# Optimization experiments

Measured on AMD Instinct MI355X. Metric: run time of the kernel, lower is better.

The kernel has to match this reference:

```python
import jax, jax.numpy as jnp
import numpy as np

H = 4096          # hidden_size
I = 14336         # intermediate_size
G = 128           # quantization group size along the input dim


def dequant(q, s, g=G):
    """Dequantize group-scaled int4 weights.
    q: [out, in] int (values in [-8, 7]); s: [out, in//g] float scales.
    Returns fp weight [out, in]: W[o, i] = q[o, i] * s[o, i // g].
    """
    O, In = q.shape
    return (q.reshape(O, In // g, g).astype(s.dtype) * s[:, :, None]).reshape(O, In)


def setup_inputs() -> dict:
    key = jax.random.key(0)
    ks = jax.random.split(key, 7)
    x = jax.random.normal(ks[0], (2, 2048, H), dtype=jnp.float32)

    def mk_qlinear(kq, ksc, out_d, in_d):
        q = jax.random.randint(kq, (out_d, in_d), -8, 8, dtype=jnp.int32)  # int4 range
        s = jax.random.uniform(ksc, (out_d, in_d // G), dtype=jnp.float32,
                               minval=0.005, maxval=0.02)
        return q, s

    gate_q, gate_s = mk_qlinear(ks[1], ks[2], I, H)
    up_q, up_s = mk_qlinear(ks[3], ks[4], I, H)
    down_q, down_s = mk_qlinear(ks[5], ks[6], H, I)
    return {"x": x,
            "gate_q": gate_q, "gate_s": gate_s,
            "up_q": up_q, "up_s": up_s,
            "down_q": down_q, "down_s": down_s}


def reference(x, gate_q, gate_s, up_q, up_s, down_q, down_s):
    # SwiGLU MLP: down( silu(gate(x)) * up(x) ) with group-dequantized weights.
    Wg = dequant(gate_q, gate_s)   # [I, H]
    Wu = dequant(up_q, up_s)       # [I, H]
    Wd = dequant(down_q, down_s)   # [H, I]
    gate_score = jax.nn.silu(jnp.einsum('bsh,ih->bsi', x, Wg))
    intermediate = gate_score * jnp.einsum('bsh,ih->bsi', x, Wu)
    return jnp.einsum('bsi,hi->bsh', intermediate, Wd)
```

## Files before the change

kernel.cpp:

```cpp
#include <hip/hip_runtime.h>
#include <hip/hip_bf16.h>


#define HDIM 4096
#define IDIM 14336
#define MTOK 4096
#define GRP 128

typedef __attribute__((ext_vector_type(8))) short bf16x8;
typedef __attribute__((ext_vector_type(4))) float f32x4;
typedef __attribute__((ext_vector_type(4))) unsigned short u16x4;

#define WAIT_LGKM0 asm volatile("s_waitcnt lgkmcnt(0)" ::: "memory")
#define WAIT_VM(N) asm volatile("s_waitcnt vmcnt(" #N ")" ::: "memory")
#define SBAR       __builtin_amdgcn_s_barrier()
#define SCHB       __builtin_amdgcn_sched_barrier(0)

__device__ __forceinline__ unsigned short f2bf(float f) {
  union { float f; unsigned int u; } v; v.f = f;
  return (unsigned short)((v.u + 0x7fffu + ((v.u >> 16) & 1u)) >> 16);
}
__device__ __forceinline__ unsigned pk2(float a, float b) {
  union { float f; unsigned u; } ua, ub; ua.f = a; ub.f = b;
  return __builtin_amdgcn_perm(ub.u, ua.u, 0x07060302u);
}

#define GLD16(G, L)                                                           \
  __builtin_amdgcn_global_load_lds(                                           \
      (const __attribute__((address_space(1))) unsigned int*)(G),             \
      (__attribute__((address_space(3))) unsigned int*)(L), 16, 0, 0)

__global__ __launch_bounds__(256) void cvt_x_kernel(const float* __restrict__ x,
                                                    unsigned short* __restrict__ xb) {
  const int n = MTOK * HDIM;
  const int stride = gridDim.x * 256 * 4;
  for (int i = (blockIdx.x * 256 + threadIdx.x) * 4; i < n; i += stride) {
    float4 v = *reinterpret_cast<const float4*>(x + i);
    u16x4 o;
    o[0] = f2bf(v.x); o[1] = f2bf(v.y); o[2] = f2bf(v.z); o[3] = f2bf(v.w);
    *reinterpret_cast<u16x4*>(xb + i) = o;
  }
}

__global__ __launch_bounds__(256) void deq_kernel(const int* __restrict__ q,
                                                  const float* __restrict__ s,
                                                  unsigned short* __restrict__ w,
                                                  int In) {
  const int row  = blockIdx.y;
  const int col0 = blockIdx.x * 2048 + threadIdx.x * 8;
  const long base = (long)row * In + col0;
  const float sc = s[row * (In / GRP) + (col0 >> 7)];
  const int4* p = (const int4*)(q + base);
  int4 a0 = p[0], a1 = p[1];
  uint4 o;
  o.x = pk2((float)a0.x * sc, (float)a0.y * sc);
  o.y = pk2((float)a0.z * sc, (float)a0.w * sc);
  o.z = pk2((float)a1.x * sc, (float)a1.y * sc);
  o.w = pk2((float)a1.z * sc, (float)a1.w * sc);
  *(uint4*)(w + base) = o;
}

__global__ __launch_bounds__(512, 2) void gateup_bf16(
    const unsigned short* __restrict__ xb,
    const unsigned short* __restrict__ wg,
    const unsigned short* __restrict__ wu,
    unsigned short* __restrict__ inter)
{
  __shared__ unsigned short As[3 * 256 * 64];
  __shared__ unsigned short Bgs[2 * 128 * 64];
  __shared__ unsigned short Bus[2 * 128 * 64];

  const int tid = threadIdx.x, lane = tid & 63, wid = tid >> 6;
  const int wm = wid >> 1, wn = wid & 1;
  const int p = blockIdx.x;
  const int l = (p & 7) * 224 + (p >> 3);
  const int m0 = (l & 15) * 256, n0 = (l >> 4) * 128;
  const int lr = lane & 15, lc = lane >> 4;

  const int ra   = tid >> 3;
  const int scol = ((tid & 7) ^ (ra & 7)) << 3;
  const unsigned short* pa  = xb + (long)(m0 + ra) * HDIM + scol;
  const unsigned short* pbg = wg + (long)(n0 + ra) * HDIM + scol;
  const unsigned short* pbu = wu + (long)(n0 + ra) * HDIM + scol;

#define A1(KT, BUF, IT)                                                       \
  GLD16(pa + (long)(IT) * 64 * HDIM + (long)(KT) * 64,                        \
        (unsigned short*)As + (BUF) * 16384 + (IT) * 4096 + wid * 512)
#define BG1(KT, BUF, IT)                                                      \
  GLD16(pbg + (long)(IT) * 64 * HDIM + (long)(KT) * 64,                       \
        (unsigned short*)Bgs + (BUF) * 8192 + (IT) * 4096 + wid * 512)
#define BU1(KT, BUF, IT)                                                      \
  GLD16(pbu + (long)(IT) * 64 * HDIM + (long)(KT) * 64,                       \
        (unsigned short*)Bus + (BUF) * 8192 + (IT) * 4096 + wid * 512)

  f32x4 accg[4][4], accu[4][4];
  const f32x4 zero = {0.f, 0.f, 0.f, 0.f};
#pragma unroll
  for (int i = 0; i < 4; ++i)
#pragma unroll
    for (int j = 0; j < 4; ++j) { accg[i][j] = zero; accu[i][j] = zero; }

  A1(0, 0, 0); A1(0, 0, 1); A1(0, 0, 2); A1(0, 0, 3);
  SCHB;
  BG1(0, 0, 0); BG1(0, 0, 1); BU1(0, 0, 0); BU1(0, 0, 1);
  SCHB;
  A1(1, 1, 0); A1(1, 1, 1); A1(1, 1, 2); A1(1, 1, 3);
  SCHB;

  const int NK = HDIM / 64;
#pragma unroll 1
  for (int kt = 0; kt < NK; ++kt) {
    WAIT_VM(4);
    SCHB;
    SBAR;
    SCHB;
    const unsigned short* Ab  = (const unsigned short*)As  + (kt % 3) * 16384;
    const unsigned short* Bgb = (const unsigned short*)Bgs + (kt & 1) * 8192;
    const unsigned short* Bub = (const unsigned short*)Bus + (kt & 1) * 8192;
    const int ktb = (kt + 1 < NK) ? kt + 1 : NK - 1;
    const int wrb = (kt + 1) & 1;
    const int kta = (kt + 2 < NK) ? kt + 2 : NK - 1;
    const int wra = (kt + 2) % 3;
    const int soff0 = (lc ^ (lr & 7)) << 3;
    const int soff1 = ((4 + lc) ^ (lr & 7)) << 3;
    bf16x8 af[4], bfr[4];

#pragma unroll
    for (int mi = 0; mi < 4; ++mi)
      af[mi] = *(const bf16x8*)&Ab[(wm * 64 + mi * 16 + lr) * 64 + soff0];
#pragma unroll
    for (int ni = 0; ni < 4; ++ni)
      bfr[ni] = *(const bf16x8*)&Bgb[(wn * 64 + ni * 16 + lr) * 64 + soff0];
    BG1(ktb, wrb, 0); BG1(ktb, wrb, 1);
    SCHB; SBAR; WAIT_LGKM0; SCHB;
    __builtin_amdgcn_s_setprio(1);
#pragma unroll
    for (int ni = 0; ni < 4; ++ni)
#pragma unroll
      for (int mi = 0; mi < 4; ++mi)
        accg[mi][ni] = __builtin_amdgcn_mfma_f32_16x16x32_bf16(af[mi], bfr[ni], accg[mi][ni], 0, 0, 0);
    __builtin_amdgcn_s_setprio(0);

#pragma unroll
    for (int ni = 0; ni < 4; ++ni)
      bfr[ni] = *(const bf16x8*)&Bub[(wn * 64 + ni * 16 + lr) * 64 + soff0];
    BU1(ktb, wrb, 0); BU1(ktb, wrb, 1);
    SCHB; SBAR; WAIT_LGKM0; SCHB;
    __builtin_amdgcn_s_setprio(1);
#pragma unroll
    for (int ni = 0; ni < 4; ++ni)
#pragma unroll
      for (int mi = 0; mi < 4; ++mi)
        accu[mi][ni] = __builtin_amdgcn_mfma_f32_16x16x32_bf16(af[mi], bfr[ni], accu[mi][ni], 0, 0, 0);
    __builtin_amdgcn_s_setprio(0);

#pragma unroll
    for (int mi = 0; mi < 4; ++mi)
      af[mi] = *(const bf16x8*)&Ab[(wm * 64 + mi * 16 + lr) * 64 + soff1];
#pragma unroll
    for (int ni = 0; ni < 4; ++ni)
      bfr[ni] = *(const bf16x8*)&Bgb[(wn * 64 + ni * 16 + lr) * 64 + soff1];
    A1(kta, wra, 0); A1(kta, wra, 1);
    SCHB; SBAR; WAIT_LGKM0; SCHB;
    __builtin_amdgcn_s_setprio(1);
#pragma unroll
    for (int ni = 0; ni < 4; ++ni)
#pragma unroll
      for (int mi = 0; mi < 4; ++mi)
        accg[mi][ni] = __builtin_amdgcn_mfma_f32_16x16x32_bf16(af[mi], bfr[ni], accg[mi][ni], 0, 0, 0);
    __builtin_amdgcn_s_setprio(0);

#pragma unroll
    for (int ni = 0; ni < 4; ++ni)
      bfr[ni] = *(const bf16x8*)&Bub[(wn * 64 + ni * 16 + lr) * 64 + soff1];
    A1(kta, wra, 2); A1(kta, wra, 3);
    SCHB; SBAR; WAIT_LGKM0; SCHB;
    __builtin_amdgcn_s_setprio(1);
#pragma unroll
    for (int ni = 0; ni < 4; ++ni)
#pragma unroll
      for (int mi = 0; mi < 4; ++mi)
        accu[mi][ni] = __builtin_amdgcn_mfma_f32_16x16x32_bf16(af[mi], bfr[ni], accu[mi][ni], 0, 0, 0);
    __builtin_amdgcn_s_setprio(0);
    SCHB;
  }

  const int r0 = m0 + wm * 64, c0 = n0 + wn * 64;
#pragma unroll
  for (int mi = 0; mi < 4; ++mi)
#pragma unroll
    for (int ni = 0; ni < 4; ++ni)
#pragma unroll
      for (int r = 0; r < 4; ++r) {
        float g = accg[mi][ni][r], u = accu[mi][ni][r];
        float sv = g / (1.f + __expf(-g));
        int row = r0 + mi * 16 + lc * 4 + r;
        int col = c0 + ni * 16 + lr;
        inter[(long)row * IDIM + col] = f2bf(sv * u);
      }
#undef A1
#undef BG1
#undef BU1
}

__global__ __launch_bounds__(512, 2) void down_bf16(
    const unsigned short* __restrict__ inter,
    const unsigned short* __restrict__ wd,
    float* __restrict__ out)
{
  __shared__ unsigned short As[2 * 256 * 64];
  __shared__ unsigned short Bs[2 * 256 * 64];

  const int tid = threadIdx.x, lane = tid & 63, wid = tid >> 6;
  const int wm = wid >> 2, wn = wid & 3;
  const int p = blockIdx.x;
  const int l = (p & 7) * 32 + (p >> 3);
  const int m0 = (l & 15) * 256, n0 = (l >> 4) * 256;
  const int lr = lane & 15, lc = lane >> 4;

  const int ra   = tid >> 3;
  const int scol = ((tid & 7) ^ (ra & 7)) << 3;
  const unsigned short* pa = inter + (long)(m0 + ra) * IDIM + scol;
  const unsigned short* pb = wd + (long)(n0 + ra) * IDIM + scol;

#define DA1(KT, BUF, IT)                                                      \
  GLD16(pa + (long)(IT) * 64 * IDIM + (long)(KT) * 64,                        \
        (unsigned short*)As + (BUF) * 16384 + (IT) * 4096 + wid * 512)
#define DB1(KT, BUF, IT)                                                      \
  GLD16(pb + (long)(IT) * 64 * IDIM + (long)(KT) * 64,                        \
        (unsigned short*)Bs + (BUF) * 16384 + (IT) * 4096 + wid * 512)

  f32x4 acc[8][4];
  const f32x4 zero = {0.f, 0.f, 0.f, 0.f};
#pragma unroll
  for (int i = 0; i < 8; ++i)
#pragma unroll
    for (int j = 0; j < 4; ++j) acc[i][j] = zero;

  DB1(0, 0, 0); DB1(0, 0, 1); DB1(0, 0, 2); DB1(0, 0, 3);
  DA1(0, 0, 0); DA1(0, 0, 1); DA1(0, 0, 2); DA1(0, 0, 3);
  SCHB;
  WAIT_VM(0);
  SBAR;
  SCHB;

  const int NK = IDIM / 64;
#pragma unroll 1
  for (int kt = 0; kt < NK; ++kt) {
    const int RD = kt & 1, WR = RD ^ 1;
    const int ktn = (kt + 1 < NK) ? kt + 1 : NK - 1;
    const unsigned short* Ab = (const unsigned short*)As + RD * 16384;
    const unsigned short* Bb = (const unsigned short*)Bs + RD * 16384;
    const int soff0 = (lc ^ (lr & 7)) << 3;
    const int soff1 = ((4 + lc) ^ (lr & 7)) << 3;
    bf16x8 af[8], bfr[4];

#pragma unroll
    for (int mi = 0; mi < 8; ++mi)
      af[mi] = *(const bf16x8*)&Ab[(wm * 128 + mi * 16 + lr) * 64 + soff0];
#pragma unroll
    for (int ni = 0; ni < 4; ++ni)
      bfr[ni] = *(const bf16x8*)&Bb[(wn * 64 + ni * 16 + lr) * 64 + soff0];
    DB1(ktn, WR, 0); DB1(ktn, WR, 1); DB1(ktn, WR, 2); DB1(ktn, WR, 3);
    SCHB; WAIT_LGKM0; SCHB;
    __builtin_amdgcn_s_setprio(1);
#pragma unroll
    for (int ni = 0; ni < 4; ++ni)
#pragma unroll
      for (int mi = 0; mi < 8; ++mi)
        acc[mi][ni] = __builtin_amdgcn_mfma_f32_16x16x32_bf16(af[mi], bfr[ni], acc[mi][ni], 0, 0, 0);
    __builtin_amdgcn_s_setprio(0);

#pragma unroll
    for (int mi = 0; mi < 8; ++mi)
      af[mi] = *(const bf16x8*)&Ab[(wm * 128 + mi * 16 + lr) * 64 + soff1];
#pragma unroll
    for (int ni = 0; ni < 4; ++ni)
      bfr[ni] = *(const bf16x8*)&Bb[(wn * 64 + ni * 16 + lr) * 64 + soff1];
    DA1(ktn, WR, 0); DA1(ktn, WR, 1); DA1(ktn, WR, 2); DA1(ktn, WR, 3);
    SCHB; WAIT_LGKM0; SCHB;
    __builtin_amdgcn_s_setprio(1);
#pragma unroll
    for (int ni = 0; ni < 4; ++ni)
#pragma unroll
      for (int mi = 0; mi < 8; ++mi)
        acc[mi][ni] = __builtin_amdgcn_mfma_f32_16x16x32_bf16(af[mi], bfr[ni], acc[mi][ni], 0, 0, 0);
    __builtin_amdgcn_s_setprio(0);

    SCHB;
    WAIT_VM(0);
    SBAR;
    SCHB;
  }

  const int r0 = m0 + wm * 128, c0 = n0 + wn * 64;
#pragma unroll
  for (int mi = 0; mi < 8; ++mi)
#pragma unroll
    for (int ni = 0; ni < 4; ++ni)
#pragma unroll
      for (int r = 0; r < 4; ++r) {
        int row = r0 + mi * 16 + lc * 4 + r;
        int col = c0 + ni * 16 + lr;
        out[(long)row * HDIM + col] = acc[mi][ni][r];
      }
#undef DA1
#undef DB1
}

extern "C" void kernel_launch(void* const* d_in, const int* in_sizes, int n_in,
                              void* d_out, int out_size, void* d_ws, size_t ws_size,
                              hipStream_t stream) {
  const float* x   = (const float*)d_in[0];
  const int*   gq  = (const int*)d_in[1];
  const float* gsc = (const float*)d_in[2];
  const int*   uq  = (const int*)d_in[3];
  const float* usc = (const float*)d_in[4];
  const int*   dq  = (const int*)d_in[5];
  const float* dsc = (const float*)d_in[6];
  float* out = (float*)d_out;

  unsigned short* xb    = (unsigned short*)d_ws;
  unsigned short* inter = xb + (size_t)MTOK * HDIM;
  unsigned short* wgb   = inter + (size_t)MTOK * IDIM;
  unsigned short* wub   = wgb + (size_t)IDIM * HDIM;

  hipLaunchKernelGGL(cvt_x_kernel, dim3(2048), dim3(256), 0, stream, x, xb);
  hipLaunchKernelGGL(deq_kernel, dim3(HDIM / 2048, IDIM), dim3(256), 0, stream,
                     gq, gsc, wgb, HDIM);
  hipLaunchKernelGGL(deq_kernel, dim3(HDIM / 2048, IDIM), dim3(256), 0, stream,
                     uq, usc, wub, HDIM);
  hipLaunchKernelGGL(gateup_bf16, dim3(1792), dim3(512), 0, stream,
                     xb, wgb, wub, inter);
  hipLaunchKernelGGL(deq_kernel, dim3(IDIM / 2048, HDIM), dim3(256), 0, stream,
                     dq, dsc, wgb, IDIM);
  hipLaunchKernelGGL(down_bf16, dim3(256), dim3(512), 0, stream,
                     inter, wgb, out);
}
```

Baseline: 1.412 ms.

## Switch gate/up GEMM to double-buffered A with one barrier per k-step

Replaces the triple-buffered A and staggered prefetch pipeline in the gate/up kernel with plain double buffering. Each k-step now has one wait-for-all plus one barrier instead of four barriers, and gate and up fragments are loaded together so their MFMAs interleave. This cuts barrier overhead and LDS use, which could allow higher occupancy. The cost is that the full vmcnt(0) wait at the end of every iteration leaves less prefetch depth to hide global-load latency.

```diff
diff --git a/kernel.cpp b/kernel.cpp
--- a/kernel.cpp
+++ b/kernel.cpp
@@ -66,7 +66,7 @@
     const unsigned short* __restrict__ wu,
     unsigned short* __restrict__ inter)
 {
-  __shared__ unsigned short As[3 * 256 * 64];
+  __shared__ unsigned short As[2 * 256 * 64];
   __shared__ unsigned short Bgs[2 * 128 * 64];
   __shared__ unsigned short Bus[2 * 128 * 64];
 
@@ -100,88 +100,68 @@
 #pragma unroll
     for (int j = 0; j < 4; ++j) { accg[i][j] = zero; accu[i][j] = zero; }
 
+  BG1(0, 0, 0); BG1(0, 0, 1); BU1(0, 0, 0); BU1(0, 0, 1);
   A1(0, 0, 0); A1(0, 0, 1); A1(0, 0, 2); A1(0, 0, 3);
   SCHB;
-  BG1(0, 0, 0); BG1(0, 0, 1); BU1(0, 0, 0); BU1(0, 0, 1);
-  SCHB;
-  A1(1, 1, 0); A1(1, 1, 1); A1(1, 1, 2); A1(1, 1, 3);
+  WAIT_VM(0);
+  SBAR;
   SCHB;
 
   const int NK = HDIM / 64;
 #pragma unroll 1
   for (int kt = 0; kt < NK; ++kt) {
-    WAIT_VM(4);
-    SCHB;
-    SBAR;
-    SCHB;
-    const unsigned short* Ab  = (const unsigned short*)As  + (kt % 3) * 16384;
-    const unsigned short* Bgb = (const unsigned short*)Bgs + (kt & 1) * 8192;
-    const unsigned short* Bub = (const unsigned short*)Bus + (kt & 1) * 8192;
-    const int ktb = (kt + 1 < NK) ? kt + 1 : NK - 1;
-    const int wrb = (kt + 1) & 1;
-    const int kta = (kt + 2 < NK) ? kt + 2 : NK - 1;
-    const int wra = (kt + 2) % 3;
+    const int RD = kt & 1, WR = RD ^ 1;
+    const int ktn = (kt + 1 < NK) ? kt + 1 : NK - 1;
+    const unsigned short* Ab  = (const unsigned short*)As  + RD * 16384;
+    const unsigned short* Bgb = (const unsigned short*)Bgs + RD * 8192;
+    const unsigned short* Bub = (const unsigned short*)Bus + RD * 8192;
     const int soff0 = (lc ^ (lr & 7)) << 3;
     const int soff1 = ((4 + lc) ^ (lr & 7)) << 3;
-    bf16x8 af[4], bfr[4];
+    bf16x8 af[4], bg[4], bu[4];
 
 #pragma unroll
     for (int mi = 0; mi < 4; ++mi)
       af[mi] = *(const bf16x8*)&Ab[(wm * 64 + mi * 16 + lr) * 64 + soff0];
 #pragma unroll
-    for (int ni = 0; ni < 4; ++ni)
-      bfr[ni] = *(const bf16x8*)&Bgb[(wn * 64 + ni * 16 + lr) * 64 + soff0];
-    BG1(ktb, wrb, 0); BG1(ktb, wrb, 1);
-    SCHB; SBAR; WAIT_LGKM0; SCHB;
+    for (int ni = 0; ni < 4; ++ni) {
+      bg[ni] = *(const bf16x8*)&Bgb[(wn * 64 + ni * 16 + lr) * 64 + soff0];
+      bu[ni] = *(const bf16x8*)&Bub[(wn * 64 + ni * 16 + lr) * 64 + soff0];
+    }
+    BG1(ktn, WR, 0); BG1(ktn, WR, 1); BU1(ktn, WR, 0); BU1(ktn, WR, 1);
+    SCHB; WAIT_LGKM0; SCHB;
     __builtin_amdgcn_s_setprio(1);
 #pragma unroll
     for (int ni = 0; ni < 4; ++ni)
 #pragma unroll
-      for (int mi = 0; mi < 4; ++mi)
-        accg[mi][ni] = __builtin_amdgcn_mfma_f32_16x16x32_bf16(af[mi], bfr[ni], accg[mi][ni], 0, 0, 0);
-    __builtin_amdgcn_s_setprio(0);
-
-#pragma unroll
-    for (int ni = 0; ni < 4; ++ni)
-      bfr[ni] = *(const bf16x8*)&Bub[(wn * 64 + ni * 16 + lr) * 64 + soff0];
-    BU1(ktb, wrb, 0); BU1(ktb, wrb, 1);
-    SCHB; SBAR; WAIT_LGKM0; SCHB;
-    __builtin_amdgcn_s_setprio(1);
-#pragma unroll
-    for (int ni = 0; ni < 4; ++ni)
-#pragma unroll
-      for (int mi = 0; mi < 4; ++mi)
-        accu[mi][ni] = __builtin_amdgcn_mfma_f32_16x16x32_bf16(af[mi], bfr[ni], accu[mi][ni], 0, 0, 0);
+      for (int mi = 0; mi < 4; ++mi) {
+        accg[mi][ni] = __builtin_amdgcn_mfma_f32_16x16x32_bf16(af[mi], bg[ni], accg[mi][ni], 0, 0, 0);
+        accu[mi][ni] = __builtin_amdgcn_mfma_f32_16x16x32_bf16(af[mi], bu[ni], accu[mi][ni], 0, 0, 0);
+      }
     __builtin_amdgcn_s_setprio(0);
 
 #pragma unroll
     for (int mi = 0; mi < 4; ++mi)
       af[mi] = *(const bf16x8*)&Ab[(wm * 64 + mi * 16 + lr) * 64 + soff1];
 #pragma unroll
-    for (int ni = 0; ni < 4; ++ni)
-      bfr[ni] = *(const bf16x8*)&Bgb[(wn * 64 + ni * 16 + lr) * 64 + soff1];
-    A1(kta, wra, 0); A1(kta, wra, 1);
-    SCHB; SBAR; WAIT_LGKM0; SCHB;
+    for (int ni = 0; ni < 4; ++ni) {
+      bg[ni] = *(const bf16x8*)&Bgb[(wn * 64 + ni * 16 + lr) * 64 + soff1];
+      bu[ni] = *(const bf16x8*)&Bub[(wn * 64 + ni * 16 + lr) * 64 + soff1];
+    }
+    A1(ktn, WR, 0); A1(ktn, WR, 1); A1(ktn, WR, 2); A1(ktn, WR, 3);
+    SCHB; WAIT_LGKM0; SCHB;
     __builtin_amdgcn_s_setprio(1);
 #pragma unroll
     for (int ni = 0; ni < 4; ++ni)
 #pragma unroll
-      for (int mi = 0; mi < 4; ++mi)
-        accg[mi][ni] = __builtin_amdgcn_mfma_f32_16x16x32_bf16(af[mi], bfr[ni], accg[mi][ni], 0, 0, 0);
+      for (int mi = 0; mi < 4; ++mi) {
+        accg[mi][ni] = __builtin_amdgcn_mfma_f32_16x16x32_bf16(af[mi], bg[ni], accg[mi][ni], 0, 0, 0);
+        accu[mi][ni] = __builtin_amdgcn_mfma_f32_16x16x32_bf16(af[mi], bu[ni], accu[mi][ni], 0, 0, 0);
+      }
     __builtin_amdgcn_s_setprio(0);
 
-#pragma unroll
-    for (int ni = 0; ni < 4; ++ni)
-      bfr[ni] = *(const bf16x8*)&Bub[(wn * 64 + ni * 16 + lr) * 64 + soff1];
-    A1(kta, wra, 2); A1(kta, wra, 3);
-    SCHB; SBAR; WAIT_LGKM0; SCHB;
-    __builtin_amdgcn_s_setprio(1);
-#pragma unroll
-    for (int ni = 0; ni < 4; ++ni)
-#pragma unroll
-      for (int mi = 0; mi < 4; ++mi)
-        accu[mi][ni] = __builtin_amdgcn_mfma_f32_16x16x32_bf16(af[mi], bfr[ni], accu[mi][ni], 0, 0, 0);
-    __builtin_amdgcn_s_setprio(0);
+    SCHB;
+    WAIT_VM(0);
+    SBAR;
     SCHB;
   }
 
```

Result: no change. 1.387 ms (-1.7%).
